# Kernel optimization log

Hardware: AMD Instinct MI355X
Metric: run time of the kernel (lower is better)

The kernel has to match this reference:

```python
import jax, jax.numpy as jnp
import numpy as np

N_TASKS = 3
N_SHARED = 4
N_TASK = 2
INP = 1024
EXPERT_DIM = 512


def setup_inputs() -> dict:
    key = jax.random.key(0)
    ks = jax.random.split(key, 7)
    s = 0.02
    task_inputs = jax.random.normal(ks[0], (N_TASKS, 16384, INP), dtype=jnp.float32)
    shared_W = jax.random.normal(ks[1], (N_SHARED, INP, EXPERT_DIM), dtype=jnp.float32) * s
    shared_b = jnp.zeros((N_SHARED, EXPERT_DIM), dtype=jnp.float32)
    task_W = jax.random.normal(ks[2], (N_TASKS, N_TASK, INP, EXPERT_DIM), dtype=jnp.float32) * s
    task_b = jnp.zeros((N_TASKS, N_TASK, EXPERT_DIM), dtype=jnp.float32)
    gate_W = jax.random.normal(ks[3], (N_TASKS, INP, N_SHARED + N_TASK), dtype=jnp.float32) * s
    gate_b = jnp.zeros((N_TASKS, N_SHARED + N_TASK), dtype=jnp.float32)
    return {
        'task_inputs': task_inputs,
        'shared_W': shared_W, 'shared_b': shared_b,
        'task_W': task_W, 'task_b': task_b,
        'gate_W': gate_W, 'gate_b': gate_b,
    }


def reference(task_inputs, shared_W, shared_b, task_W, task_b, gate_W, gate_b):
    # task_inputs: [T, B, I]
    x0 = task_inputs[0]  # shared experts always see task 0's input
    # shared experts: [B, E_s, O]
    shared_outs = jax.nn.relu(jnp.einsum('bi,eio->beo', x0, shared_W) + shared_b)
    # per-task experts: [T, B, E_t, O]
    task_outs = jax.nn.relu(jnp.einsum('tbi,teio->tbeo', task_inputs, task_W) + task_b[:, None, :, :])
    # stack shared + task experts -> [T, B, E_s+E_t, O]
    T = task_inputs.shape[0]
    all_outs = jnp.concatenate([
        jnp.broadcast_to(shared_outs[None], (T,) + shared_outs.shape),
        task_outs,
    ], axis=2)
    # gates: softmax over experts, [T, B, E_s+E_t]
    g = jax.nn.softmax(jnp.einsum('tbi,tig->tbg', task_inputs, gate_W) + gate_b[:, None, :], axis=-1)
    # gated weighted sum over experts -> [T, B, O]
    return jnp.einsum('tbeo,tbe->tbo', all_outs, g)
```

## Files before the change

kernel.cpp:

```cpp
#include <hip/hip_runtime.h>
#include <hip/hip_bf16.h>
#include <stdint.h>


#define TTASKS 3
#define BROWS  16384
#define KDIM   1024
#define ODIM   512
#define NGATE  6

typedef __attribute__((ext_vector_type(8))) __bf16 bf16x8;
typedef __attribute__((ext_vector_type(4))) float  f32x4;

#define XB_OFF 0
#define WT_OFF 100663296UL
#define GT_OFF 111149056UL
#define SH_OFF 112328704UL

__global__ __launch_bounds__(256) void cvt_inputs(const float* __restrict__ x,
                                                  __bf16* __restrict__ xb) {
  size_t i = ((size_t)blockIdx.x * 256 + threadIdx.x) * 8;
  const float4* p = (const float4*)(x + i);
  float4 a = p[0], b = p[1];
  bf16x8 o = { (__bf16)a.x, (__bf16)a.y, (__bf16)a.z, (__bf16)a.w,
               (__bf16)b.x, (__bf16)b.y, (__bf16)b.z, (__bf16)b.w };
  *(bf16x8*)(xb + i) = o;
}

__global__ __launch_bounds__(256) void cvt_weights(const float* __restrict__ shW,
                                                   const float* __restrict__ tkW,
                                                   __bf16* __restrict__ wT) {
  int s = blockIdx.z;
  const float* src = (s < 4) ? (shW + (size_t)s * KDIM * ODIM)
                             : (tkW + (size_t)(s - 4) * KDIM * ODIM);
  int o   = blockIdx.x * 64 + (threadIdx.x & 63);
  int sub = threadIdx.x >> 6;
#pragma unroll
  for (int kk = 0; kk < 2; ++kk) {
    int k0 = blockIdx.y * 64 + (sub * 2 + kk) * 8;
    bf16x8 v;
#pragma unroll
    for (int i = 0; i < 8; ++i)
      v[i] = (__bf16)src[(size_t)(k0 + i) * ODIM + o];
    *(bf16x8*)(wT + ((size_t)s * ODIM + o) * KDIM + k0) = v;
  }
}

__global__ __launch_bounds__(256) void gates_kernel(const float* __restrict__ x,
                                                    const float* __restrict__ gW,
                                                    const float* __restrict__ gb,
                                                    float* __restrict__ gates) {
  int w = blockIdx.x * 4 + (threadIdx.x >> 6);
  int lane = threadIdx.x & 63;
  int t = w >> 14, b = w & (BROWS - 1);
  const float* xr = x + ((size_t)t * BROWS + b) * KDIM;
  const float* gw = gW + (size_t)t * KDIM * NGATE;
  float d[NGATE] = {0.f, 0.f, 0.f, 0.f, 0.f, 0.f};
  for (int i = 0; i < 16; ++i) {
    int k = i * 64 + lane;
    float xv = xr[k];
#pragma unroll
    for (int j = 0; j < NGATE; ++j) d[j] += xv * gw[k * NGATE + j];
  }
#pragma unroll
  for (int j = 0; j < NGATE; ++j) {
#pragma unroll
    for (int off = 32; off > 0; off >>= 1) d[j] += __shfl_xor(d[j], off, 64);
    d[j] += gb[t * NGATE + j];
  }
  float m = d[0];
#pragma unroll
  for (int j = 1; j < NGATE; ++j) m = fmaxf(m, d[j]);
  float s = 0.f;
#pragma unroll
  for (int j = 0; j < NGATE; ++j) { d[j] = expf(d[j] - m); s += d[j]; }
  float inv = 1.f / s;
  if (lane < NGATE) {
    float v = d[0];
#pragma unroll
    for (int j = 1; j < NGATE; ++j) v = (lane == j) ? d[j] : v;
    gates[(size_t)w * NGATE + lane] = v * inv;
  }
}

__device__ __forceinline__ void gemm_128x128(const __bf16* __restrict__ Aptr,
                                             const __bf16* __restrict__ Bptr,
                                             __bf16* As, __bf16* Bs,
                                             f32x4 acc[4][4]) {
  const int tid = threadIdx.x;
  const int lane = tid & 63;
  const int wv = tid >> 6;
  const int wm = wv >> 1, wn = wv & 1;
  const int lr = lane & 15, lg = lane >> 4;

  for (int kt = 0; kt < 16; ++kt) {
    const int k0 = kt * 64;
#pragma unroll
    for (int it = 0; it < 4; ++it) {
      int idx = it * 256 + tid;
      int r   = idx >> 3;
      int c8  = (idx & 7) << 3;
      __builtin_amdgcn_global_load_lds(
          (const __attribute__((address_space(1))) void*)(Aptr + (size_t)r * KDIM + k0 + c8),
          (__attribute__((address_space(3))) void*)(As + (it * 256 + wv * 64) * 8), 16, 0, 0);
      __builtin_amdgcn_global_load_lds(
          (const __attribute__((address_space(1))) void*)(Bptr + (size_t)r * KDIM + k0 + c8),
          (__attribute__((address_space(3))) void*)(Bs + (it * 256 + wv * 64) * 8), 16, 0, 0);
    }
    __syncthreads();

    const __bf16* aB = As + (wm * 64 + lr) * 64 + lg * 8;
    const __bf16* bB = Bs + (wn * 64 + lr) * 64 + lg * 8;
#pragma unroll
    for (int ks = 0; ks < 2; ++ks) {
      bf16x8 af[4], bf[4];
#pragma unroll
      for (int m = 0; m < 4; ++m) af[m] = *(const bf16x8*)(aB + m * 1024 + ks * 32);
#pragma unroll
      for (int n = 0; n < 4; ++n) bf[n] = *(const bf16x8*)(bB + n * 1024 + ks * 32);
#pragma unroll
      for (int m = 0; m < 4; ++m)
#pragma unroll
        for (int n = 0; n < 4; ++n)
          acc[m][n] = __builtin_amdgcn_mfma_f32_16x16x32_bf16(af[m], bf[n], acc[m][n], 0, 0, 0);
    }
    __syncthreads();
  }
}

__global__ __launch_bounds__(256, 2) void shared_gemm(const __bf16* __restrict__ xb0,
                                                      const __bf16* __restrict__ wT,
                                                      const float* __restrict__ shb,
                                                      __bf16* __restrict__ shOut) {
  __shared__ __bf16 As[128 * 64], Bs[128 * 64];
  const int e = blockIdx.z;
  const int rowBase = blockIdx.x * 128, colBase = blockIdx.y * 128;
  const int tid = threadIdx.x, lane = tid & 63, wv = tid >> 6;
  const int wm = wv >> 1, wn = wv & 1, lr = lane & 15, lg = lane >> 4;

  f32x4 acc[4][4];
  f32x4 z = {0.f, 0.f, 0.f, 0.f};
#pragma unroll
  for (int m = 0; m < 4; ++m)
#pragma unroll
    for (int n = 0; n < 4; ++n) acc[m][n] = z;

  gemm_128x128(xb0 + (size_t)rowBase * KDIM,
               wT + ((size_t)e * ODIM + colBase) * KDIM, As, Bs, acc);

#pragma unroll
  for (int n = 0; n < 4; ++n) {
    int col = colBase + wn * 64 + n * 16 + lr;
    float bias = shb[e * ODIM + col];
#pragma unroll
    for (int m = 0; m < 4; ++m)
#pragma unroll
      for (int r = 0; r < 4; ++r) {
        int row = rowBase + wm * 64 + m * 16 + lg * 4 + r;
        float v = fmaxf(acc[m][n][r] + bias, 0.f);
        shOut[((size_t)e * BROWS + row) * ODIM + col] = (__bf16)v;
      }
  }
}

__global__ __launch_bounds__(256, 2) void task_gemm(const __bf16* __restrict__ xb,
                                                    const __bf16* __restrict__ wT,
                                                    const float* __restrict__ tkb,
                                                    const float* __restrict__ gates,
                                                    const __bf16* __restrict__ shOut,
                                                    float* __restrict__ out) {
  __shared__ __bf16 As[128 * 64], Bs[128 * 64];
  const int t = blockIdx.z;
  const int rowBase = blockIdx.x * 128, colBase = blockIdx.y * 128;
  const int tid = threadIdx.x, lane = tid & 63, wv = tid >> 6;
  const int wm = wv >> 1, wn = wv & 1, lr = lane & 15, lg = lane >> 4;

  float outv[4][4][4];

#pragma unroll
  for (int m = 0; m < 4; ++m)
#pragma unroll
    for (int r = 0; r < 4; ++r) {
      int row = rowBase + wm * 64 + m * 16 + lg * 4 + r;
      const float* gp = gates + ((size_t)t * BROWS + row) * NGATE;
      float g0 = gp[0], g1 = gp[1], g2 = gp[2], g3 = gp[3];
#pragma unroll
      for (int n = 0; n < 4; ++n) {
        int col = colBase + wn * 64 + n * 16 + lr;
        size_t rc = (size_t)row * ODIM + col;
        float s = g0 * (float)shOut[rc]
                + g1 * (float)shOut[(size_t)BROWS * ODIM + rc]
                + g2 * (float)shOut[2 * (size_t)BROWS * ODIM + rc]
                + g3 * (float)shOut[3 * (size_t)BROWS * ODIM + rc];
        outv[m][n][r] = s;
      }
    }

#pragma unroll 1
  for (int j = 0; j < 2; ++j) {
    f32x4 acc[4][4];
    f32x4 z = {0.f, 0.f, 0.f, 0.f};
#pragma unroll
    for (int m = 0; m < 4; ++m)
#pragma unroll
      for (int n = 0; n < 4; ++n) acc[m][n] = z;

    gemm_128x128(xb + ((size_t)t * BROWS + rowBase) * KDIM,
                 wT + ((size_t)(4 + t * 2 + j) * ODIM + colBase) * KDIM, As, Bs, acc);

#pragma unroll
    for (int n = 0; n < 4; ++n) {
      int col = colBase + wn * 64 + n * 16 + lr;
      float bias = tkb[(t * 2 + j) * ODIM + col];
#pragma unroll
      for (int m = 0; m < 4; ++m)
#pragma unroll
        for (int r = 0; r < 4; ++r) {
          int row = rowBase + wm * 64 + m * 16 + lg * 4 + r;
          float g = gates[((size_t)t * BROWS + row) * NGATE + 4 + j];
          outv[m][n][r] += g * fmaxf(acc[m][n][r] + bias, 0.f);
        }
    }
  }

#pragma unroll
  for (int n = 0; n < 4; ++n) {
    int col = colBase + wn * 64 + n * 16 + lr;
#pragma unroll
    for (int m = 0; m < 4; ++m)
#pragma unroll
      for (int r = 0; r < 4; ++r) {
        int row = rowBase + wm * 64 + m * 16 + lg * 4 + r;
        out[((size_t)t * BROWS + row) * ODIM + col] = outv[m][n][r];
      }
  }
}

extern "C" void kernel_launch(void* const* d_in, const int* in_sizes, int n_in,
                              void* d_out, int out_size, void* d_ws, size_t ws_size,
                              hipStream_t stream) {
  const float* x   = (const float*)d_in[0];
  const float* shW = (const float*)d_in[1];
  const float* shb = (const float*)d_in[2];
  const float* tkW = (const float*)d_in[3];
  const float* tkb = (const float*)d_in[4];
  const float* gW  = (const float*)d_in[5];
  const float* gb  = (const float*)d_in[6];
  float* out = (float*)d_out;
  (void)in_sizes; (void)n_in; (void)out_size; (void)ws_size;

  char* ws = (char*)d_ws;
  __bf16* xb    = (__bf16*)(ws + XB_OFF);
  __bf16* wT    = (__bf16*)(ws + WT_OFF);
  float*  gates = (float*) (ws + GT_OFF);
  __bf16* shOut = (__bf16*)(ws + SH_OFF);

  cvt_inputs <<<dim3(24576), 256, 0, stream>>>(x, xb);
  cvt_weights<<<dim3(8, 16, 10), 256, 0, stream>>>(shW, tkW, wT);
  gates_kernel<<<dim3((TTASKS * BROWS) / 4), 256, 0, stream>>>(x, gW, gb, gates);

  shared_gemm<<<dim3(BROWS / 128, ODIM / 128, 4), 256, 0, stream>>>(xb, wT, shb, shOut);

  task_gemm<<<dim3(BROWS / 128, ODIM / 128, TTASKS), 256, 0, stream>>>(xb, wT, tkb, gates,
                                                                       shOut, out);
}
```

Measured before the change: 677.1 us.

## Swizzle LDS tiles, split task GEMM into two kernels, gates from bf16 inputs

Applies an XOR swizzle to the LDS tile layout so that MFMA fragment reads avoid bank conflicts. The task GEMM, which looped over two experts per block, becomes two kernels. The first writes the shared-expert mix plus the first task expert, and the second adds the second expert into the output with a read-modify-write. The gates kernel now reads the bf16-converted inputs with vector loads instead of fp32, halving its input traffic but computing the gate logits from rounded inputs.

```diff
diff --git a/kernel.cpp b/kernel.cpp
--- a/kernel.cpp
+++ b/kernel.cpp
@@ -16,6 +16,8 @@
 #define WT_OFF 100663296UL
 #define GT_OFF 111149056UL
 #define SH_OFF 112328704UL
+
+#define MFMA_(a, bb, c) __builtin_amdgcn_mfma_f32_16x16x32_bf16(a, bb, c, 0, 0, 0)
 
 __global__ __launch_bounds__(256) void cvt_inputs(const float* __restrict__ x,
                                                   __bf16* __restrict__ xb) {
@@ -46,21 +48,26 @@
   }
 }
 
-__global__ __launch_bounds__(256) void gates_kernel(const float* __restrict__ x,
+__global__ __launch_bounds__(256) void gates_kernel(const __bf16* __restrict__ xb,
                                                     const float* __restrict__ gW,
                                                     const float* __restrict__ gb,
                                                     float* __restrict__ gates) {
   int w = blockIdx.x * 4 + (threadIdx.x >> 6);
   int lane = threadIdx.x & 63;
   int t = w >> 14, b = w & (BROWS - 1);
-  const float* xr = x + ((size_t)t * BROWS + b) * KDIM;
+  const __bf16* xr = xb + ((size_t)t * BROWS + b) * KDIM;
   const float* gw = gW + (size_t)t * KDIM * NGATE;
   float d[NGATE] = {0.f, 0.f, 0.f, 0.f, 0.f, 0.f};
-  for (int i = 0; i < 16; ++i) {
-    int k = i * 64 + lane;
-    float xv = xr[k];
-#pragma unroll
-    for (int j = 0; j < NGATE; ++j) d[j] += xv * gw[k * NGATE + j];
+#pragma unroll
+  for (int i = 0; i < 2; ++i) {
+    int k0 = (i * 64 + lane) * 8;
+    bf16x8 xv = *(const bf16x8*)(xr + k0);
+#pragma unroll
+    for (int kk = 0; kk < 8; ++kk) {
+      float xf = (float)xv[kk];
+#pragma unroll
+      for (int j = 0; j < NGATE; ++j) d[j] += xf * gw[(k0 + kk) * NGATE + j];
+    }
   }
 #pragma unroll
   for (int j = 0; j < NGATE; ++j) {
@@ -83,46 +90,45 @@
   }
 }
 
-__device__ __forceinline__ void gemm_128x128(const __bf16* __restrict__ Aptr,
-                                             const __bf16* __restrict__ Bptr,
-                                             __bf16* As, __bf16* Bs,
-                                             f32x4 acc[4][4]) {
-  const int tid = threadIdx.x;
-  const int lane = tid & 63;
-  const int wv = tid >> 6;
+__device__ __forceinline__ void gemm_128(const __bf16* __restrict__ Ap,
+                                         const __bf16* __restrict__ Bp,
+                                         __bf16* As, __bf16* Bs,
+                                         f32x4 acc[4][4]) {
+  const int tid = threadIdx.x, lane = tid & 63, wv = tid >> 6;
   const int wm = wv >> 1, wn = wv & 1;
-  const int lr = lane & 15, lg = lane >> 4;
+  const int lr = lane & 15, lg = lane >> 4, x7 = lr & 7;
 
   for (int kt = 0; kt < 16; ++kt) {
     const int k0 = kt * 64;
 #pragma unroll
     for (int it = 0; it < 4; ++it) {
-      int idx = it * 256 + tid;
-      int r   = idx >> 3;
-      int c8  = (idx & 7) << 3;
+      const int idx = it * 256 + tid;
+      const int r   = idx >> 3;
+      const int cs  = (idx & 7) ^ (r & 7);
       __builtin_amdgcn_global_load_lds(
-          (const __attribute__((address_space(1))) void*)(Aptr + (size_t)r * KDIM + k0 + c8),
+          (const __attribute__((address_space(1))) void*)(Ap + (size_t)r * KDIM + k0 + cs * 8),
           (__attribute__((address_space(3))) void*)(As + (it * 256 + wv * 64) * 8), 16, 0, 0);
       __builtin_amdgcn_global_load_lds(
-          (const __attribute__((address_space(1))) void*)(Bptr + (size_t)r * KDIM + k0 + c8),
+          (const __attribute__((address_space(1))) void*)(Bp + (size_t)r * KDIM + k0 + cs * 8),
           (__attribute__((address_space(3))) void*)(Bs + (it * 256 + wv * 64) * 8), 16, 0, 0);
     }
     __syncthreads();
 
-    const __bf16* aB = As + (wm * 64 + lr) * 64 + lg * 8;
-    const __bf16* bB = Bs + (wn * 64 + lr) * 64 + lg * 8;
+    const __bf16* aB = As + (wm * 64 + lr) * 64;
+    const __bf16* bB = Bs + (wn * 64 + lr) * 64;
 #pragma unroll
     for (int ks = 0; ks < 2; ++ks) {
+      const int xo = ((ks * 4 + lg) ^ x7) * 8;
       bf16x8 af[4], bf[4];
 #pragma unroll
-      for (int m = 0; m < 4; ++m) af[m] = *(const bf16x8*)(aB + m * 1024 + ks * 32);
-#pragma unroll
-      for (int n = 0; n < 4; ++n) bf[n] = *(const bf16x8*)(bB + n * 1024 + ks * 32);
-#pragma unroll
-      for (int m = 0; m < 4; ++m)
-#pragma unroll
-        for (int n = 0; n < 4; ++n)
-          acc[m][n] = __builtin_amdgcn_mfma_f32_16x16x32_bf16(af[m], bf[n], acc[m][n], 0, 0, 0);
+      for (int mi = 0; mi < 4; ++mi) af[mi] = *(const bf16x8*)(aB + mi * 16 * 64 + xo);
+#pragma unroll
+      for (int ni = 0; ni < 4; ++ni) bf[ni] = *(const bf16x8*)(bB + ni * 16 * 64 + xo);
+#pragma unroll
+      for (int mi = 0; mi < 4; ++mi)
+#pragma unroll
+        for (int ni = 0; ni < 4; ++ni)
+          acc[mi][ni] = MFMA_(af[mi], bf[ni], acc[mi][ni]);
     }
     __syncthreads();
   }
@@ -132,7 +138,7 @@
                                                       const __bf16* __restrict__ wT,
                                                       const float* __restrict__ shb,
                                                       __bf16* __restrict__ shOut) {
-  __shared__ __bf16 As[128 * 64], Bs[128 * 64];
+  __shared__ __align__(16) __bf16 As[128 * 64], Bs[128 * 64];
   const int e = blockIdx.z;
   const int rowBase = blockIdx.x * 128, colBase = blockIdx.y * 128;
   const int tid = threadIdx.x, lane = tid & 63, wv = tid >> 6;
@@ -141,99 +147,106 @@
   f32x4 acc[4][4];
   f32x4 z = {0.f, 0.f, 0.f, 0.f};
 #pragma unroll
-  for (int m = 0; m < 4; ++m)
-#pragma unroll
-    for (int n = 0; n < 4; ++n) acc[m][n] = z;
-
-  gemm_128x128(xb0 + (size_t)rowBase * KDIM,
-               wT + ((size_t)e * ODIM + colBase) * KDIM, As, Bs, acc);
-
-#pragma unroll
-  for (int n = 0; n < 4; ++n) {
-    int col = colBase + wn * 64 + n * 16 + lr;
+  for (int mi = 0; mi < 4; ++mi)
+#pragma unroll
+    for (int ni = 0; ni < 4; ++ni) acc[mi][ni] = z;
+
+  gemm_128(xb0 + (size_t)rowBase * KDIM,
+           wT + ((size_t)e * ODIM + colBase) * KDIM, As, Bs, acc);
+
+#pragma unroll
+  for (int ni = 0; ni < 4; ++ni) {
+    int col = colBase + wn * 64 + ni * 16 + lr;
     float bias = shb[e * ODIM + col];
 #pragma unroll
-    for (int m = 0; m < 4; ++m)
+    for (int mi = 0; mi < 4; ++mi)
 #pragma unroll
       for (int r = 0; r < 4; ++r) {
-        int row = rowBase + wm * 64 + m * 16 + lg * 4 + r;
-        float v = fmaxf(acc[m][n][r] + bias, 0.f);
+        int row = rowBase + wm * 64 + mi * 16 + lg * 4 + r;
+        float v = fmaxf(acc[mi][ni][r] + bias, 0.f);
         shOut[((size_t)e * BROWS + row) * ODIM + col] = (__bf16)v;
       }
   }
 }
 
-__global__ __launch_bounds__(256, 2) void task_gemm(const __bf16* __restrict__ xb,
-                                                    const __bf16* __restrict__ wT,
-                                                    const float* __restrict__ tkb,
-                                                    const float* __restrict__ gates,
-                                                    const __bf16* __restrict__ shOut,
-                                                    float* __restrict__ out) {
-  __shared__ __bf16 As[128 * 64], Bs[128 * 64];
+__global__ __launch_bounds__(256, 2) void taskA_gemm(const __bf16* __restrict__ xb,
+                                                     const __bf16* __restrict__ wT,
+                                                     const float* __restrict__ tkb,
+                                                     const float* __restrict__ gates,
+                                                     const __bf16* __restrict__ shOut,
+                                                     float* __restrict__ out) {
+  __shared__ __align__(16) __bf16 As[128 * 64], Bs[128 * 64];
   const int t = blockIdx.z;
   const int rowBase = blockIdx.x * 128, colBase = blockIdx.y * 128;
   const int tid = threadIdx.x, lane = tid & 63, wv = tid >> 6;
   const int wm = wv >> 1, wn = wv & 1, lr = lane & 15, lg = lane >> 4;
-
-  float outv[4][4][4];
-
-#pragma unroll
-  for (int m = 0; m < 4; ++m)
+  const size_t NB = (size_t)BROWS * ODIM;
+
+  f32x4 acc[4][4];
+  f32x4 z = {0.f, 0.f, 0.f, 0.f};
+#pragma unroll
+  for (int mi = 0; mi < 4; ++mi)
+#pragma unroll
+    for (int ni = 0; ni < 4; ++ni) acc[mi][ni] = z;
+
+  gemm_128(xb + ((size_t)t * BROWS + rowBase) * KDIM,
+           wT + ((size_t)(4 + t * 2) * ODIM + colBase) * KDIM, As, Bs, acc);
+
+#pragma unroll
+  for (int mi = 0; mi < 4; ++mi)
 #pragma unroll
     for (int r = 0; r < 4; ++r) {
-      int row = rowBase + wm * 64 + m * 16 + lg * 4 + r;
+      int row = rowBase + wm * 64 + mi * 16 + lg * 4 + r;
       const float* gp = gates + ((size_t)t * BROWS + row) * NGATE;
-      float g0 = gp[0], g1 = gp[1], g2 = gp[2], g3 = gp[3];
-#pragma unroll
-      for (int n = 0; n < 4; ++n) {
-        int col = colBase + wn * 64 + n * 16 + lr;
+      float g0 = gp[0], g1 = gp[1], g2 = gp[2], g3 = gp[3], g4 = gp[4];
+#pragma unroll
+      for (int ni = 0; ni < 4; ++ni) {
+        int col = colBase + wn * 64 + ni * 16 + lr;
         size_t rc = (size_t)row * ODIM + col;
-        float s = g0 * (float)shOut[rc]
-                + g1 * (float)shOut[(size_t)BROWS * ODIM + rc]
-                + g2 * (float)shOut[2 * (size_t)BROWS * ODIM + rc]
-                + g3 * (float)shOut[3 * (size_t)BROWS * ODIM + rc];
-        outv[m][n][r] = s;
+        float s = g0 * (float)shOut[rc] + g1 * (float)shOut[NB + rc] +
+                  g2 * (float)shOut[2 * NB + rc] + g3 * (float)shOut[3 * NB + rc];
+        float bias = tkb[(t * 2) * ODIM + col];
+        s += g4 * fmaxf(acc[mi][ni][r] + bias, 0.f);
+        out[((size_t)t * BROWS + row) * ODIM + col] = s;
       }
     }
-
-#pragma unroll 1
-  for (int j = 0; j < 2; ++j) {
-    f32x4 acc[4][4];
-    f32x4 z = {0.f, 0.f, 0.f, 0.f};
-#pragma unroll
-    for (int m = 0; m < 4; ++m)
-#pragma unroll
-      for (int n = 0; n < 4; ++n) acc[m][n] = z;
-
-    gemm_128x128(xb + ((size_t)t * BROWS + rowBase) * KDIM,
-                 wT + ((size_t)(4 + t * 2 + j) * ODIM + colBase) * KDIM, As, Bs, acc);
-
-#pragma unroll
-    for (int n = 0; n < 4; ++n) {
-      int col = colBase + wn * 64 + n * 16 + lr;
-      float bias = tkb[(t * 2 + j) * ODIM + col];
-#pragma unroll
-      for (int m = 0; m < 4; ++m)
-#pragma unroll
-        for (int r = 0; r < 4; ++r) {
-          int row = rowBase + wm * 64 + m * 16 + lg * 4 + r;
-          float g = gates[((size_t)t * BROWS + row) * NGATE + 4 + j];
-          outv[m][n][r] += g * fmaxf(acc[m][n][r] + bias, 0.f);
-        }
-    }
-  }
-
-#pragma unroll
-  for (int n = 0; n < 4; ++n) {
-    int col = colBase + wn * 64 + n * 16 + lr;
-#pragma unroll
-    for (int m = 0; m < 4; ++m)
-#pragma unroll
-      for (int r = 0; r < 4; ++r) {
-        int row = rowBase + wm * 64 + m * 16 + lg * 4 + r;
-        out[((size_t)t * BROWS + row) * ODIM + col] = outv[m][n][r];
+}
+
+__global__ __launch_bounds__(256, 2) void taskB_gemm(const __bf16* __restrict__ xb,
+                                                     const __bf16* __restrict__ wT,
+                                                     const float* __restrict__ tkb,
+                                                     const float* __restrict__ gates,
+                                                     float* __restrict__ out) {
+  __shared__ __align__(16) __bf16 As[128 * 64], Bs[128 * 64];
+  const int t = blockIdx.z;
+  const int rowBase = blockIdx.x * 128, colBase = blockIdx.y * 128;
+  const int tid = threadIdx.x, lane = tid & 63, wv = tid >> 6;
+  const int wm = wv >> 1, wn = wv & 1, lr = lane & 15, lg = lane >> 4;
+
+  f32x4 acc[4][4];
+  f32x4 z = {0.f, 0.f, 0.f, 0.f};
+#pragma unroll
+  for (int mi = 0; mi < 4; ++mi)
+#pragma unroll
+    for (int ni = 0; ni < 4; ++ni) acc[mi][ni] = z;
+
+  gemm_128(xb + ((size_t)t * BROWS + rowBase) * KDIM,
+           wT + ((size_t)(4 + t * 2 + 1) * ODIM + colBase) * KDIM, As, Bs, acc);
+
+#pragma unroll
+  for (int mi = 0; mi < 4; ++mi)
+#pragma unroll
+    for (int r = 0; r < 4; ++r) {
+      int row = rowBase + wm * 64 + mi * 16 + lg * 4 + r;
+      float g5 = gates[((size_t)t * BROWS + row) * NGATE + 5];
+#pragma unroll
+      for (int ni = 0; ni < 4; ++ni) {
+        int col = colBase + wn * 64 + ni * 16 + lr;
+        float bias = tkb[(t * 2 + 1) * ODIM + col];
+        size_t oi = ((size_t)t * BROWS + row) * ODIM + col;
+        out[oi] += g5 * fmaxf(acc[mi][ni][r] + bias, 0.f);
       }
-  }
+    }
 }
 
 extern "C" void kernel_launch(void* const* d_in, const int* in_sizes, int n_in,
@@ -257,10 +270,11 @@
 
   cvt_inputs <<<dim3(24576), 256, 0, stream>>>(x, xb);
   cvt_weights<<<dim3(8, 16, 10), 256, 0, stream>>>(shW, tkW, wT);
-  gates_kernel<<<dim3((TTASKS * BROWS) / 4), 256, 0, stream>>>(x, gW, gb, gates);
+  gates_kernel<<<dim3((TTASKS * BROWS) / 4), 256, 0, stream>>>(xb, gW, gb, gates);
 
   shared_gemm<<<dim3(BROWS / 128, ODIM / 128, 4), 256, 0, stream>>>(xb, wT, shb, shOut);
-
-  task_gemm<<<dim3(BROWS / 128, ODIM / 128, TTASKS), 256, 0, stream>>>(xb, wT, tkb, gates,
-                                                                       shOut, out);
-}
+  taskA_gemm <<<dim3(BROWS / 128, ODIM / 128, TTASKS), 256, 0, stream>>>(xb, wT, tkb, gates,
+                                                                         shOut, out);
+  taskB_gemm <<<dim3(BROWS / 128, ODIM / 128, TTASKS), 256, 0, stream>>>(xb, wT, tkb, gates,
+                                                                         out);
+}
```

After: 649.6 us. -4.1%, faster.
